# Performance work log

Hardware: AMD Instinct MI355X
Metric: run time of the kernel (lower is better)

## Reference

```python
import jax, jax.numpy as jnp
import numpy as np

L = 6        # gnn_layers
H = 4        # heads
C = 128      # per-head channels = hidden // heads
HID = 512    # hidden
IN = 768     # in_dim
N = 20000    # nodes
E = 320000   # edges
P = 100000   # scored pairs


def _gelu(v):
    return jax.nn.gelu(v, approximate=False)


def _ln(v, g, b):
    m = v.mean(-1, keepdims=True)
    var = v.var(-1, keepdims=True)
    return (v - m) / jnp.sqrt(var + 1e-5) * g + b


def setup_inputs() -> dict:
    key = jax.random.key(0)
    ks = jax.random.split(key, 24)
    g = lambda k, shape, s=0.02: (jax.random.normal(k, shape, jnp.float32) * s)
    inp = {}
    inp["x"] = jax.random.normal(ks[0], (N, IN), jnp.float32)
    inp["edge_index"] = jax.random.randint(ks[1], (2, E), 0, N)
    inp["edges"] = jax.random.randint(ks[2], (2, P), 0, N)
    # FeatureMixer (no alt branch)
    inp["mixer_W"] = g(ks[3], (IN, HID)); inp["mixer_b"] = jnp.zeros((HID,), jnp.float32)
    # Stacked TransformerConv params per layer
    inp["Wq"] = g(ks[4], (L, HID, HID)); inp["bq"] = jnp.zeros((L, HID), jnp.float32)
    inp["Wk"] = g(ks[5], (L, HID, HID)); inp["bk"] = jnp.zeros((L, HID), jnp.float32)
    inp["Wv"] = g(ks[6], (L, HID, HID)); inp["bv"] = jnp.zeros((L, HID), jnp.float32)
    inp["Ws"] = g(ks[7], (L, HID, HID)); inp["bs"] = jnp.zeros((L, HID), jnp.float32)  # lin_skip (root weight)
    inp["ln_g"] = jnp.ones((L, HID), jnp.float32); inp["ln_b"] = jnp.zeros((L, HID), jnp.float32)
    # Dual projections
    inp["syn_W"] = g(ks[8], (HID, HID)); inp["syn_b"] = jnp.zeros((HID,), jnp.float32)
    inp["ant_W"] = g(ks[9], (HID, HID)); inp["ant_b"] = jnp.zeros((HID,), jnp.float32)
    # Bilinear score matrices
    inp["W_syn"] = g(ks[10], (HID, HID), 0.04)
    inp["W_ant"] = g(ks[11], (HID, HID), 0.04)
    # Gate MLP: Linear(4*HID, HID) -> GELU -> Linear(HID, 1) -> Sigmoid
    inp["gW1"] = g(ks[12], (4 * HID, HID)); inp["gb1"] = jnp.zeros((HID,), jnp.float32)
    inp["gW2"] = g(ks[13], (HID, 1)); inp["gb2"] = jnp.zeros((1,), jnp.float32)
    return inp


def reference(x, edge_index, edges, mixer_W, mixer_b, Wq, bq, Wk, bk, Wv, bv,
              Ws, bs, ln_g, ln_b, syn_W, syn_b, ant_W, ant_b, W_syn, W_ant,
              gW1, gb1, gW2, gb2):
    src, dst = edge_index[0], edge_index[1]
    scale = 1.0 / np.sqrt(C).astype(np.float32)
    # FeatureMixer (eval mode: dropout = identity)
    h = _gelu(x @ mixer_W + mixer_b)  # [N, HID]
    for l in range(L):
        # node-side projections, then gather per edge
        q = (h @ Wq[l] + bq[l]).reshape(N, H, C)
        k = (h @ Wk[l] + bk[l]).reshape(N, H, C)
        v = (h @ Wv[l] + bv[l]).reshape(N, H, C)
        logits = (q[dst] * k[src]).sum(-1) * scale          # [E, H]
        mx = jax.ops.segment_max(logits, dst, num_segments=N)   # [N, H]
        ex = jnp.exp(logits - mx[dst])
        den = jax.ops.segment_sum(ex, dst, num_segments=N)      # [N, H]
        alpha = ex / den[dst]                                   # segment softmax over incoming edges
        msg = alpha[..., None] * v[src]                         # [E, H, C]
        out = jax.ops.segment_sum(msg, dst, num_segments=N).reshape(N, HID)
        out = out + h @ Ws[l] + bs[l]                           # root/skip term of TransformerConv
        out = _gelu(out)
        h = _ln(h + out, ln_g[l], ln_b[l])
    z_syn = _gelu(h @ syn_W + syn_b)
    z_ant = _gelu(h @ ant_W + ant_b)
    i, j = edges[0], edges[1]
    vi_s, vj_s = z_syn[i], z_syn[j]
    vi_a, vj_a = z_ant[i], z_ant[j]
    s_syn = ((vi_s @ W_syn) * vj_s).sum(-1)
    s_ant = ((vi_a @ W_ant) * vj_a).sum(-1)
    pair = jnp.concatenate([jnp.abs(vi_s - vj_s), vi_s * vj_s,
                            jnp.abs(vi_a - vj_a), vi_a * vj_a], axis=-1)  # [P, 4*HID]
    g = jax.nn.sigmoid(_gelu(pair @ gW1 + gb1) @ gW2 + gb2).squeeze(-1)
    return g * s_ant + (1.0 - g) * (-s_syn)
```

## Files before the change

### kernel.cpp

```cpp
#include <hip/hip_runtime.h>
#include <cstdint>

#define L_LAYERS 6

typedef __attribute__((ext_vector_type(8))) short bf16x8;
typedef __attribute__((ext_vector_type(4))) float f32x4;
typedef __attribute__((ext_vector_type(2))) float f32x2;

__device__ __forceinline__ float gelu1(float v) {
    return 0.5f * v * (1.0f + erff(v * 0.7071067811865475f));
}

__device__ __forceinline__ unsigned int f2bf2(float a, float b) {
    union { float f; unsigned u; } x, y;
    x.f = a; y.f = b;
    unsigned lo = (x.u + 0x7FFFu + ((x.u >> 16) & 1u)) >> 16;
    unsigned hi = (y.u + 0x7FFFu + ((y.u >> 16) & 1u)) & 0xFFFF0000u;
    return lo | hi;
}

__device__ __forceinline__ unsigned short f2bf1(float a) {
    union { float f; unsigned u; } x;
    x.f = a;
    return (unsigned short)((x.u + 0x7FFFu + ((x.u >> 16) & 1u)) >> 16);
}

__device__ __forceinline__ unsigned cvt_pk_bf16(float lo, float hi) {
    unsigned r;
    asm("v_cvt_pk_bf16_f32 %0, %1, %2" : "=v"(r) : "v"(lo), "v"(hi));
    return r;
}

__device__ __forceinline__ float2 bfp2(unsigned u) {
    union { unsigned u; float f; } a, b;
    a.u = u << 16;
    b.u = u & 0xFFFF0000u;
    return make_float2(a.f, b.f);
}

__device__ __forceinline__ void gload16(const void* g, void* l) {
    __builtin_amdgcn_global_load_lds(
        (const __attribute__((address_space(1))) void*)g,
        (__attribute__((address_space(3))) void*)l, 16, 0, 0);
}


__global__ void k_zero(int* __restrict__ p, int n) {
    int i = blockIdx.x * 256 + threadIdx.x;
    if (i < n) p[i] = 0;
}


__global__ void k_hist(const int* __restrict__ dst, int* __restrict__ hist, int E) {
    int e = blockIdx.x * 256 + threadIdx.x;
    if (e < E) atomicAdd(&hist[dst[e]], 1);
}

__global__ __launch_bounds__(1024) void k_scan(const int* __restrict__ hist,
                                               int* __restrict__ off, int n) {
    __shared__ int buf[1024];
    __shared__ int carry;
    int tid = threadIdx.x;
    if (tid == 0) carry = 0;
    __syncthreads();
    for (int base = 0; base < n; base += 1024) {
        int v = (base + tid < n) ? hist[base + tid] : 0;
        buf[tid] = v;
        __syncthreads();
        int x = v;
        for (int o = 1; o < 1024; o <<= 1) {
            int t = (tid >= o) ? buf[tid - o] : 0;
            __syncthreads();
            x += t;
            buf[tid] = x;
            __syncthreads();
        }
        int c = carry;
        if (base + tid < n) off[base + tid] = c + x - v;
        __syncthreads();
        if (tid == 1023) carry = c + buf[1023];
        __syncthreads();
    }
    if (tid == 0) off[n] = carry;
}

__global__ void k_scatter(const int* __restrict__ src, const int* __restrict__ dst,
                          const int* __restrict__ off, int* __restrict__ cursor,
                          int* __restrict__ srcS, int E) {
    int e = blockIdx.x * 256 + threadIdx.x;
    if (e < E) {
        int d = dst[e];
        int pos = off[d] + atomicAdd(&cursor[d], 1);
        srcS[pos] = src[e];
    }
}


__global__ void k_wcat(const float* __restrict__ Wq, const float* __restrict__ Wk,
                       const float* __restrict__ Wv, const float* __restrict__ Ws,
                       short* __restrict__ Wt) {
    int idx = blockIdx.x * 256 + threadIdx.x;
    int k = idx & 511;
    int nf = (idx >> 9) & 2047;
    int l = idx >> 20;
    int sel = nf >> 9, nn = nf & 511;
    const float* W = (sel == 0) ? Wq : (sel == 1) ? Wk : (sel == 2) ? Wv : Ws;
    float v = W[((size_t)l * 512 + k) * 512 + nn];
    Wt[idx] = (short)f2bf1(v);
}

__global__ void k_tr(const float* __restrict__ W, short* __restrict__ Wt, int K, int N,
                     int swz) {
    int k = blockIdx.x * 256 + threadIdx.x;
    int n = blockIdx.y;
    if (k < K) {
        int kk = k;
        if (swz) kk = (k & ~31) | (((((k >> 3) & 3) ^ ((n >> 1) & 3))) << 3) | (k & 7);
        Wt[(size_t)n * K + kk] = (short)f2bf1(W[(size_t)k * N + n]);
    }
}

__global__ void k_bcat(const float* __restrict__ bq, const float* __restrict__ bk,
                       const float* __restrict__ bv, const float* __restrict__ bs,
                       float* __restrict__ bcat) {
    int idx = blockIdx.x * 256 + threadIdx.x;
    if (idx >= L_LAYERS * 2048) return;
    int l = idx >> 11, n = idx & 2047;
    int sel = n >> 9, nn = n & 511;
    const float* b = (sel == 0) ? bq : (sel == 1) ? bk : (sel == 2) ? bv : bs;
    bcat[idx] = b[l * 512 + nn];
}

__global__ void k_bdual(const float* __restrict__ sb, const float* __restrict__ ab,
                        float* __restrict__ bd) {
    int idx = blockIdx.x * 256 + threadIdx.x;
    if (idx < 1024) bd[idx] = (idx < 512) ? sb[idx] : ab[idx - 512];
}


__global__ __launch_bounds__(256) void gemm_a32(
    const float* __restrict__ A, int lda,
    const short* __restrict__ Bt,
    const float* __restrict__ bias,
    float* __restrict__ Cf, short* __restrict__ Cbf, int ldc,
    int M, int N, int K, int act) {
    __shared__ __align__(16) short As[128][40];
    __shared__ __align__(16) short Bs[128][40];
    const int tid = threadIdx.x;
    const int lane = tid & 63;
    const int wave = tid >> 6;
    const int wr = (wave >> 1) * 64;
    const int wc = (wave & 1) * 64;
    const int l16 = lane & 15;
    const int quad = lane >> 4;
    const int row0 = blockIdx.x * 128;
    const int col0 = blockIdx.y * 128;
    const int sr = tid >> 2;
    const int sk = (tid & 3) * 8;

    f32x4 acc[4][4];
#pragma unroll
    for (int i = 0; i < 4; ++i)
#pragma unroll
        for (int j = 0; j < 4; ++j)
            acc[i][j] = f32x4{0.f, 0.f, 0.f, 0.f};

    for (int kb = 0; kb < K; kb += 32) {
#pragma unroll
        for (int hh = 0; hh < 2; ++hh) {
            int r = sr + hh * 64;
            int gr = row0 + r;
            float4 a0, a1;
            if (gr < M) {
                const float* p = A + (size_t)gr * lda + kb + sk;
                a0 = *(const float4*)p;
                a1 = *(const float4*)(p + 4);
            } else {
                a0 = make_float4(0.f, 0.f, 0.f, 0.f);
                a1 = make_float4(0.f, 0.f, 0.f, 0.f);
            }
            uint4 av;
            av.x = f2bf2(a0.x, a0.y);
            av.y = f2bf2(a0.z, a0.w);
            av.z = f2bf2(a1.x, a1.y);
            av.w = f2bf2(a1.z, a1.w);
            *(uint4*)&As[r][sk] = av;
            const short* bp = Bt + (size_t)(col0 + r) * K + kb + sk;
            *(uint4*)&Bs[r][sk] = *(const uint4*)bp;
        }
        __syncthreads();
        bf16x8 af[4], bfr[4];
#pragma unroll
        for (int i = 0; i < 4; ++i)
            af[i] = *(const bf16x8*)&As[wr + i * 16 + l16][quad * 8];
#pragma unroll
        for (int j = 0; j < 4; ++j)
            bfr[j] = *(const bf16x8*)&Bs[wc + j * 16 + l16][quad * 8];
#pragma unroll
        for (int i = 0; i < 4; ++i)
#pragma unroll
            for (int j = 0; j < 4; ++j)
                acc[i][j] = __builtin_amdgcn_mfma_f32_16x16x32_bf16(af[i], bfr[j], acc[i][j], 0, 0, 0);
        __syncthreads();
    }
#pragma unroll
    for (int i = 0; i < 4; ++i) {
        int rbase = row0 + wr + i * 16 + quad * 4;
#pragma unroll
        for (int j = 0; j < 4; ++j) {
            int c = col0 + wc + j * 16 + l16;
            float bv = bias ? bias[c] : 0.0f;
#pragma unroll
            for (int rg = 0; rg < 4; ++rg) {
                int gr = rbase + rg;
                if (gr < M) {
                    float v = acc[i][j][rg] + bv;
                    if (act) v = gelu1(v);
                    Cf[(size_t)gr * ldc + c] = v;
                    if (Cbf) Cbf[(size_t)gr * ldc + c] = (short)f2bf1(v);
                }
            }
        }
    }
}


__global__ __launch_bounds__(256) void gemm_bb(
    const short* __restrict__ A, int lda,
    const short* __restrict__ Bt,
    const float* __restrict__ bias,
    short* __restrict__ C, unsigned char* __restrict__ C8, int ldc,
    int M, int N, int K, int act) {
    __shared__ __align__(16) short As[128 * 32];
    __shared__ __align__(16) short Bs[128 * 32];
    const int tid = threadIdx.x;
    const int lane = tid & 63;
    const int wave = tid >> 6;
    const int wr = (wave >> 1) * 64;
    const int wc = (wave & 1) * 64;
    const int l16 = lane & 15;
    const int quad = lane >> 4;
    const int row0 = blockIdx.x * 128;
    const int col0 = blockIdx.y * 128;
    const int c0 = tid, c1 = tid + 256;
    const int r0 = c0 >> 2, kq0 = (c0 & 3) * 8;
    const int r1 = c1 >> 2, kq1 = (c1 & 3) * 8;
    int ga0 = row0 + r0; if (ga0 >= M) ga0 = M - 1;
    int ga1 = row0 + r1; if (ga1 >= M) ga1 = M - 1;
    const short* Ap0 = A + (size_t)ga0 * lda + kq0;
    const short* Ap1 = A + (size_t)ga1 * lda + kq1;
    const short* Bp0 = Bt + (size_t)(col0 + r0) * K + kq0;
    const short* Bp1 = Bt + (size_t)(col0 + r1) * K + kq1;

    f32x4 acc[4][4];
#pragma unroll
    for (int i = 0; i < 4; ++i)
#pragma unroll
        for (int j = 0; j < 4; ++j)
            acc[i][j] = f32x4{0.f, 0.f, 0.f, 0.f};

    for (int kb = 0; kb < K; kb += 32) {
        gload16(Ap0 + kb, &As[c0 * 8]);
        gload16(Ap1 + kb, &As[c1 * 8]);
        gload16(Bp0 + kb, &Bs[c0 * 8]);
        gload16(Bp1 + kb, &Bs[c1 * 8]);
        __syncthreads();
        bf16x8 af[4], bfr[4];
#pragma unroll
        for (int i = 0; i < 4; ++i)
            af[i] = *(const bf16x8*)&As[(wr + i * 16 + l16) * 32 + quad * 8];
#pragma unroll
        for (int j = 0; j < 4; ++j)
            bfr[j] = *(const bf16x8*)&Bs[(wc + j * 16 + l16) * 32 + quad * 8];
#pragma unroll
        for (int i = 0; i < 4; ++i)
#pragma unroll
            for (int j = 0; j < 4; ++j)
                acc[i][j] = __builtin_amdgcn_mfma_f32_16x16x32_bf16(af[i], bfr[j], acc[i][j], 0, 0, 0);
        __syncthreads();
    }
#pragma unroll
    for (int i = 0; i < 4; ++i) {
        int rbase = row0 + wr + i * 16 + quad * 4;
#pragma unroll
        for (int j = 0; j < 4; ++j) {
            int c = col0 + wc + j * 16 + l16;
            float bv = bias ? bias[c] : 0.0f;
#pragma unroll
            for (int rg = 0; rg < 4; ++rg) {
                int gr = rbase + rg;
                if (gr < M) {
                    float v = acc[i][j][rg] + bv;
                    if (act) v = gelu1(v);
                    C[(size_t)gr * ldc + c] = (short)f2bf1(v);
                    if (C8) {
                        int r8 = __builtin_amdgcn_cvt_pk_fp8_f32(v, v, 0, false);
                        C8[(size_t)gr * ldc + c] = (unsigned char)(r8 & 0xFF);
                    }
                }
            }
        }
    }
}


__global__ __launch_bounds__(256) void gemm_qkvs(
    const short* __restrict__ A,
    const short* __restrict__ Bt,
    const float* __restrict__ bias,
    short* __restrict__ qvs,
    unsigned char* __restrict__ kv8,
    int M, int mtiles) {
    const int K = 512;
    const int id = blockIdx.x;
    const int xcd = id & 7;
    const int t = id >> 3;
    const int col_t = t & 15;
    const int row_t = (t >> 4) * 8 + xcd;
    if (row_t >= mtiles) return;
    const int row0 = row_t * 128;
    const int col0 = col_t * 128;
    __shared__ __align__(16) short As[128 * 32];
    __shared__ __align__(16) short Bs[128 * 32];
    const int tid = threadIdx.x;
    const int lane = tid & 63;
    const int wave = tid >> 6;
    const int wr = (wave >> 1) * 64;
    const int wc = (wave & 1) * 64;
    const int l16 = lane & 15;
    const int quad = lane >> 4;
    const int c0 = tid, c1 = tid + 256;
    const int r0 = c0 >> 2, kq0 = (c0 & 3) * 8;
    const int r1 = c1 >> 2, kq1 = (c1 & 3) * 8;
    int ga0 = row0 + r0; if (ga0 >= M) ga0 = M - 1;
    int ga1 = row0 + r1; if (ga1 >= M) ga1 = M - 1;
    const short* Ap0 = A + (size_t)ga0 * K + kq0;
    const short* Ap1 = A + (size_t)ga1 * K + kq1;
    const short* Bp0 = Bt + (size_t)(col0 + r0) * K + kq0;
    const short* Bp1 = Bt + (size_t)(col0 + r1) * K + kq1;

    f32x4 acc[4][4];
#pragma unroll
    for (int i = 0; i < 4; ++i)
#pragma unroll
        for (int j = 0; j < 4; ++j)
            acc[i][j] = f32x4{0.f, 0.f, 0.f, 0.f};

    for (int kb = 0; kb < K; kb += 32) {
        gload16(Ap0 + kb, &As[c0 * 8]);
        gload16(Ap1 + kb, &As[c1 * 8]);
        gload16(Bp0 + kb, &Bs[c0 * 8]);
        gload16(Bp1 + kb, &Bs[c1 * 8]);
        __syncthreads();
        bf16x8 af[4], bfr[4];
#pragma unroll
        for (int i = 0; i < 4; ++i)
            af[i] = *(const bf16x8*)&As[(wr + i * 16 + l16) * 32 + quad * 8];
#pragma unroll
        for (int j = 0; j < 4; ++j)
            bfr[j] = *(const bf16x8*)&Bs[(wc + j * 16 + l16) * 32 + quad * 8];
#pragma unroll
        for (int i = 0; i < 4; ++i)
#pragma unroll
            for (int j = 0; j < 4; ++j)
                acc[i][j] = __builtin_amdgcn_mfma_f32_16x16x32_bf16(af[i], bfr[j], acc[i][j], 0, 0, 0);
        __syncthreads();
    }
#pragma unroll
    for (int i = 0; i < 4; ++i) {
        int rbase = row0 + wr + i * 16 + quad * 4;
#pragma unroll
        for (int j = 0; j < 4; ++j) {
            int c = col0 + wc + j * 16 + l16;
            int sec = c >> 9;
            int cc = c & 511;
            float bv = bias[c];
#pragma unroll
            for (int rg = 0; rg < 4; ++rg) {
                int gr = rbase + rg;
                if (gr < M) {
                    float v = acc[i][j][rg] + bv;
                    if (sec == 1 || sec == 2) {
                        int r8 = __builtin_amdgcn_cvt_pk_fp8_f32(v, v, 0, false);
                        int off = (sec == 1) ? cc : 512 + cc;
                        kv8[(size_t)gr * 1024 + off] = (unsigned char)(r8 & 0xFF);
                    } else {
                        int off = (sec == 0) ? cc : 512 + cc;
                        qvs[(size_t)gr * 1024 + off] = (short)f2bf1(v);
                    }
                }
            }
        }
    }
}


__global__ __launch_bounds__(512, 2) void gemm_gate(
    const unsigned char* __restrict__ z8,
    const int* __restrict__ pi, const int* __restrict__ pj, int P,
    const short* __restrict__ Bt,
    const float* __restrict__ gb1,
    const float* __restrict__ gW2,
    float* __restrict__ gpart) {
    __shared__ __align__(16) short Bs[512 * 32];
    __shared__ __align__(16) short As[128 * 32];
    __shared__ int iArr[128];
    __shared__ int jArr[128];
    __shared__ float rowsum[128];
    const int row0 = blockIdx.x * 128;
    const int tid = threadIdx.x;
    const int lane = tid & 63;
    const int wave = tid >> 6;
    const int wm = wave >> 2;
    const int wn = wave & 3;
    const int l16 = lane & 15;
    const int quad = lane >> 4;
    const int arow = tid >> 2;
    const int aslot = tid & 3;
    const int qs = (quad ^ ((l16 >> 1) & 3)) * 8;
    const int awoff = arow * 32 + ((aslot ^ ((arow >> 1) & 3)) << 3);

    if (tid < 128) {
        int p = row0 + tid;
        int ok = (p < P);
        iArr[tid] = ok ? pi[p] : 0;
        jArr[tid] = ok ? pj[p] : 0;
        rowsum[tid] = 0.0f;
    }
    __syncthreads();
    const unsigned char* zi = z8 + (size_t)iArr[arow] * 1024 + aslot * 8;
    const unsigned char* zj = z8 + (size_t)jArr[arow] * 1024 + aslot * 8;
    const short* brow = Bt + (size_t)(tid >> 2) * 2048 + (tid & 3) * 8;

    f32x4 acc[4][8];
#pragma unroll
    for (int i = 0; i < 4; ++i)
#pragma unroll
        for (int j = 0; j < 8; ++j)
            acc[i][j] = f32x4{0.f, 0.f, 0.f, 0.f};

    uint2 xu = *(const uint2*)zi;
    uint2 yu = *(const uint2*)zj;

    for (int kc = 0; kc < 32; ++kc) {
        const int chb = ((kc >> 4) << 10) + ((kc & 15) << 5);
#pragma unroll
        for (int g = 0; g < 4; ++g)
            gload16(brow + (size_t)(g * 128) * 2048 + chb, &Bs[(g * 512 + tid) * 8]);
        uint2 xn, yn;
        if (kc + 1 < 32) {
            int koff = (((kc + 1) >> 4) << 9) + (((kc + 1) & 15) << 5);
            xn = *(const uint2*)(zi + koff);
            yn = *(const uint2*)(zj + koff);
        }
        f32x2 x0 = __builtin_amdgcn_cvt_pk_f32_fp8((int)xu.x, false);
        f32x2 x1 = __builtin_amdgcn_cvt_pk_f32_fp8((int)xu.x, true);
        f32x2 x2 = __builtin_amdgcn_cvt_pk_f32_fp8((int)xu.y, false);
        f32x2 x3 = __builtin_amdgcn_cvt_pk_f32_fp8((int)xu.y, true);
        f32x2 y0 = __builtin_amdgcn_cvt_pk_f32_fp8((int)yu.x, false);
        f32x2 y1 = __builtin_amdgcn_cvt_pk_f32_fp8((int)yu.x, true);
        f32x2 y2 = __builtin_amdgcn_cvt_pk_f32_fp8((int)yu.y, false);
        f32x2 y3 = __builtin_amdgcn_cvt_pk_f32_fp8((int)yu.y, true);
        uint4 aa, am;
        aa.x = cvt_pk_bf16(fabsf(x0.x - y0.x), fabsf(x0.y - y0.y));
        aa.y = cvt_pk_bf16(fabsf(x1.x - y1.x), fabsf(x1.y - y1.y));
        aa.z = cvt_pk_bf16(fabsf(x2.x - y2.x), fabsf(x2.y - y2.y));
        aa.w = cvt_pk_bf16(fabsf(x3.x - y3.x), fabsf(x3.y - y3.y));
        am.x = cvt_pk_bf16(x0.x * y0.x, x0.y * y0.y);
        am.y = cvt_pk_bf16(x1.x * y1.x, x1.y * y1.y);
        am.z = cvt_pk_bf16(x2.x * y2.x, x2.y * y2.y);
        am.w = cvt_pk_bf16(x3.x * y3.x, x3.y * y3.y);
        *(uint4*)&As[awoff] = aa;
        __syncthreads();
        {
            bf16x8 af[4];
#pragma unroll
            for (int i = 0; i < 4; ++i)
                af[i] = *(const bf16x8*)&As[(wm * 64 + i * 16 + l16) * 32 + qs];
#pragma unroll
            for (int j = 0; j < 8; ++j) {
                bf16x8 bf = *(const bf16x8*)&Bs[(wn * 128 + j * 16 + l16) * 32 + qs];
#pragma unroll
                for (int i = 0; i < 4; ++i)
                    acc[i][j] = __builtin_amdgcn_mfma_f32_16x16x32_bf16(af[i], bf, acc[i][j], 0, 0, 0);
            }
        }
        __syncthreads();
#pragma unroll
        for (int g = 0; g < 4; ++g)
            gload16(brow + (size_t)(g * 128) * 2048 + chb + 512, &Bs[(g * 512 + tid) * 8]);
        *(uint4*)&As[awoff] = am;
        __syncthreads();
        {
            bf16x8 af[4];
#pragma unroll
            for (int i = 0; i < 4; ++i)
                af[i] = *(const bf16x8*)&As[(wm * 64 + i * 16 + l16) * 32 + qs];
#pragma unroll
            for (int j = 0; j < 8; ++j) {
                bf16x8 bf = *(const bf16x8*)&Bs[(wn * 128 + j * 16 + l16) * 32 + qs];
#pragma unroll
                for (int i = 0; i < 4; ++i)
                    acc[i][j] = __builtin_amdgcn_mfma_f32_16x16x32_bf16(af[i], bf, acc[i][j], 0, 0, 0);
            }
        }
        __syncthreads();
        xu = xn;
        yu = yn;
    }
#pragma unroll
    for (int i = 0; i < 4; ++i) {
#pragma unroll
        for (int rg = 0; rg < 4; ++rg) {
            float partial = 0.f;
#pragma unroll
            for (int j = 0; j < 8; ++j) {
                int cc = wn * 128 + j * 16 + l16;
                partial += gelu1(acc[i][j][rg] + gb1[cc]) * gW2[cc];
            }
            partial += __shfl_xor(partial, 1);
            partial += __shfl_xor(partial, 2);
            partial += __shfl_xor(partial, 4);
            partial += __shfl_xor(partial, 8);
            if (l16 == 0)
                atomicAdd(&rowsum[wm * 64 + i * 16 + quad * 4 + rg], partial);
        }
    }
    __syncthreads();
    if (tid < 128) {
        int p = row0 + tid;
        if (p < P) gpart[p] = rowsum[tid];
    }
}


__global__ __launch_bounds__(256) void k_attn(const short* __restrict__ qvs,
                                              const unsigned char* __restrict__ kv8,
                                              const int* __restrict__ srcS,
                                              const int* __restrict__ offs,
                                              float* __restrict__ h,
                                              short* __restrict__ h_bf,
                                              const float* __restrict__ lng,
                                              const float* __restrict__ lnb, int Nn) {
    const int tid = threadIdx.x;
    const int lane = tid & 63;
    const int wv = tid >> 6;
    const int n = blockIdx.x * 4 + wv;
    if (n >= Nn) return;
    const int st = offs[n], en = offs[n + 1];
    const size_t chOff = (size_t)lane * 8;

    uint4 qv = *(const uint4*)(qvs + (size_t)n * 1024 + chOff);
    float2 q0 = bfp2(qv.x), q1 = bfp2(qv.y), q2 = bfp2(qv.z), q3 = bfp2(qv.w);
    float acc[8];
#pragma unroll
    for (int i = 0; i < 8; ++i) acc[i] = 0.f;
    float m_l = -3.4e38f, l_l = 0.f;

    for (int e0 = st; e0 < en; e0 += 64) {
        int cnt = min(64, en - e0);
        int myS = (lane < cnt) ? srcS[e0 + lane] : 0;
        for (int ei = 0; ei < cnt; ++ei) {
            int s = __shfl(myS, ei);
            const unsigned char* srow = kv8 + (size_t)s * 1024 + chOff;
            uint2 kq = *(const uint2*)srow;
            uint2 vq = *(const uint2*)(srow + 512);
            f32x2 k0 = __builtin_amdgcn_cvt_pk_f32_fp8((int)kq.x, false);
            f32x2 k1 = __builtin_amdgcn_cvt_pk_f32_fp8((int)kq.x, true);
            f32x2 k2 = __builtin_amdgcn_cvt_pk_f32_fp8((int)kq.y, false);
            f32x2 k3 = __builtin_amdgcn_cvt_pk_f32_fp8((int)kq.y, true);
            float d = q0.x * k0.x + q0.y * k0.y + q1.x * k1.x + q1.y * k1.y +
                      q2.x * k2.x + q2.y * k2.y + q3.x * k3.x + q3.y * k3.y;
            d += __shfl_xor(d, 1);
            d += __shfl_xor(d, 2);
            d += __shfl_xor(d, 4);
            d += __shfl_xor(d, 8);
            float lg = d * 0.08838834764831845f;
            float m_new = fmaxf(m_l, lg);
            float sc = __expf(m_l - m_new);
            float p = __expf(lg - m_new);
            l_l = l_l * sc + p;
            m_l = m_new;
            f32x2 v0 = __builtin_amdgcn_cvt_pk_f32_fp8((int)vq.x, false);
            f32x2 v1 = __builtin_amdgcn_cvt_pk_f32_fp8((int)vq.x, true);
            f32x2 v2 = __builtin_amdgcn_cvt_pk_f32_fp8((int)vq.y, false);
            f32x2 v3 = __builtin_amdgcn_cvt_pk_f32_fp8((int)vq.y, true);
            acc[0] = acc[0] * sc + p * v0.x; acc[1] = acc[1] * sc + p * v0.y;
            acc[2] = acc[2] * sc + p * v1.x; acc[3] = acc[3] * sc + p * v1.y;
            acc[4] = acc[4] * sc + p * v2.x; acc[5] = acc[5] * sc + p * v2.y;
            acc[6] = acc[6] * sc + p * v3.x; acc[7] = acc[7] * sc + p * v3.y;
        }
    }
    float rinv = (en > st) ? 1.0f / l_l : 0.f;
    uint4 su = *(const uint4*)(qvs + (size_t)n * 1024 + 512 + chOff);
    float2 s0 = bfp2(su.x), s1 = bfp2(su.y), s2 = bfp2(su.z), s3 = bfp2(su.w);
    float sv[8] = {s0.x, s0.y, s1.x, s1.y, s2.x, s2.y, s3.x, s3.y};
    const float* hp = h + (size_t)n * 512 + chOff;
    float4 h0 = *(const float4*)hp;
    float4 h1 = *(const float4*)(hp + 4);
    float hv[8] = {h0.x, h0.y, h0.z, h0.w, h1.x, h1.y, h1.z, h1.w};
    float r[8];
    float sum = 0.f, ssq = 0.f;
#pragma unroll
    for (int i = 0; i < 8; ++i) {
        r[i] = hv[i] + gelu1(acc[i] * rinv + sv[i]);
        sum += r[i];
        ssq += r[i] * r[i];
    }
    for (int o = 32; o; o >>= 1) {
        sum += __shfl_xor(sum, o);
        ssq += __shfl_xor(ssq, o);
    }
    float mean = sum * (1.0f / 512.0f);
    float var = ssq * (1.0f / 512.0f) - mean * mean;
    float inv = rsqrtf(var + 1e-5f);
    const float* gp = lng + chOff;
    const float* bp = lnb + chOff;
    float4 g0 = *(const float4*)gp, g1 = *(const float4*)(gp + 4);
    float4 b0 = *(const float4*)bp, b1 = *(const float4*)(bp + 4);
    float ga[8] = {g0.x, g0.y, g0.z, g0.w, g1.x, g1.y, g1.z, g1.w};
    float ba[8] = {b0.x, b0.y, b0.z, b0.w, b1.x, b1.y, b1.z, b1.w};
    float o8[8];
#pragma unroll
    for (int i = 0; i < 8; ++i) o8[i] = (r[i] - mean) * inv * ga[i] + ba[i];
    float* hw = h + (size_t)n * 512 + chOff;
    *(float4*)hw = make_float4(o8[0], o8[1], o8[2], o8[3]);
    *(float4*)(hw + 4) = make_float4(o8[4], o8[5], o8[6], o8[7]);
    uint4 ob;
    ob.x = f2bf2(o8[0], o8[1]);
    ob.y = f2bf2(o8[2], o8[3]);
    ob.z = f2bf2(o8[4], o8[5]);
    ob.w = f2bf2(o8[6], o8[7]);
    *(uint4*)(h_bf + (size_t)n * 512 + chOff) = ob;
}


__global__ __launch_bounds__(256) void k_pairscore(const short* __restrict__ z,
                                                   const short* __restrict__ t,
                                                   const int* __restrict__ pi,
                                                   const int* __restrict__ pj,
                                                   float* __restrict__ ssyn,
                                                   float* __restrict__ sant, int P) {
    int p = blockIdx.x * 4 + (threadIdx.x >> 6);
    if (p >= P) return;
    int lane = threadIdx.x & 63;
    int i = pi[p], j = pj[p];
    uint4 a = *(const uint4*)(t + (size_t)i * 1024 + lane * 8);
    uint4 b = *(const uint4*)(z + (size_t)j * 1024 + lane * 8);
    float2 a0 = bfp2(a.x), a1 = bfp2(a.y), a2 = bfp2(a.z), a3 = bfp2(a.w);
    float2 b0 = bfp2(b.x), b1 = bfp2(b.y), b2 = bfp2(b.z), b3 = bfp2(b.w);
    float ds = a0.x * b0.x + a0.y * b0.y + a1.x * b1.x + a1.y * b1.y +
               a2.x * b2.x + a2.y * b2.y + a3.x * b3.x + a3.y * b3.y;
    uint4 c = *(const uint4*)(t + (size_t)i * 1024 + 512 + lane * 8);
    uint4 d = *(const uint4*)(z + (size_t)j * 1024 + 512 + lane * 8);
    float2 c0 = bfp2(c.x), c1 = bfp2(c.y), c2 = bfp2(c.z), c3 = bfp2(c.w);
    float2 d0 = bfp2(d.x), d1 = bfp2(d.y), d2 = bfp2(d.z), d3 = bfp2(d.w);
    float da = c0.x * d0.x + c0.y * d0.y + c1.x * d1.x + c1.y * d1.y +
               c2.x * d2.x + c2.y * d2.y + c3.x * d3.x + c3.y * d3.y;
    for (int o = 32; o; o >>= 1) {
        ds += __shfl_xor(ds, o);
        da += __shfl_xor(da, o);
    }
    if (lane == 0) { ssyn[p] = ds; sant[p] = da; }
}


__global__ void k_final(const float* __restrict__ gpart, const float* __restrict__ gb2,
                        const float* __restrict__ ssyn, const float* __restrict__ sant,
                        float* __restrict__ out, int P) {
    int p = blockIdx.x * 256 + threadIdx.x;
    if (p < P) {
        float s = 1.0f / (1.0f + __expf(-(gpart[p] + gb2[0])));
        out[p] = s * sant[p] - (1.0f - s) * ssyn[p];
    }
}


extern "C" void kernel_launch(void* const* d_in, const int* in_sizes, int n_in,
                              void* d_out, int out_size, void* d_ws, size_t ws_size,
                              hipStream_t stream) {
    const float* x = (const float*)d_in[0];
    const int* ei = (const int*)d_in[1];
    const int* pe = (const int*)d_in[2];
    const float* mixer_W = (const float*)d_in[3];
    const float* mixer_b = (const float*)d_in[4];
    const float* Wq = (const float*)d_in[5];
    const float* bq = (const float*)d_in[6];
    const float* Wk = (const float*)d_in[7];
    const float* bk = (const float*)d_in[8];
    const float* Wv = (const float*)d_in[9];
    const float* bv = (const float*)d_in[10];
    const float* Ws = (const float*)d_in[11];
    const float* bs = (const float*)d_in[12];
    const float* ln_g = (const float*)d_in[13];
    const float* ln_b = (const float*)d_in[14];
    const float* syn_W = (const float*)d_in[15];
    const float* syn_b = (const float*)d_in[16];
    const float* ant_W = (const float*)d_in[17];
    const float* ant_b = (const float*)d_in[18];
    const float* W_syn = (const float*)d_in[19];
    const float* W_ant = (const float*)d_in[20];
    const float* gW1 = (const float*)d_in[21];
    const float* gb1 = (const float*)d_in[22];
    const float* gW2 = (const float*)d_in[23];
    const float* gb2 = (const float*)d_in[24];
    float* out = (float*)d_out;

    const int Nn = in_sizes[0] / 768;
    const int E = in_sizes[1] / 2;
    const int P = in_sizes[2] / 2;

    char* w = (char*)d_ws;
    auto alloc = [&](size_t bytes) -> char* {
        char* p = w;
        w += (bytes + 255) & ~(size_t)255;
        return p;
    };
    float* h = (float*)alloc((size_t)Nn * 512 * 4);
    short* h_bf = (short*)alloc((size_t)Nn * 512 * 2);
    char* U = alloc((size_t)Nn * 2048 * 2);
    short* qvs = (short*)U;
    unsigned char* kv8 = (unsigned char*)(U + (size_t)Nn * 1024 * 2);
    short* zB = (short*)U;
    short* tB = (short*)(U + (size_t)Nn * 1024 * 2);
    unsigned char* z8 = (unsigned char*)alloc((size_t)Nn * 1024);
    float* ssyn = (float*)alloc((size_t)P * 3 * 4);
    float* sant = ssyn + P;
    float* gpart = ssyn + 2 * P;
    int* srcS = (int*)alloc((size_t)E * 4);
    int* hist = (int*)alloc((size_t)Nn * 2 * 4);
    int* cursor = hist + Nn;
    int* offs = (int*)alloc((size_t)(Nn + 1) * 4);
    short* mixWt = (short*)alloc((size_t)512 * 768 * 2);
    short* wcat = (short*)alloc((size_t)L_LAYERS * 2048 * 512 * 2);
    short* dualWt = (short*)alloc((size_t)1024 * 512 * 2);
    short* bilWt = (short*)alloc((size_t)1024 * 512 * 2);
    short* gw1t = (short*)alloc((size_t)512 * 2048 * 2);
    float* bcat = (float*)alloc((size_t)L_LAYERS * 2048 * 4);
    float* bdual = (float*)alloc((size_t)1024 * 4);

    k_zero<<<(2 * Nn + 255) / 256, 256, 0, stream>>>(hist, 2 * Nn);
    k_hist<<<(E + 255) / 256, 256, 0, stream>>>(ei + E, hist, E);
    k_scan<<<1, 1024, 0, stream>>>(hist, offs, Nn);
    k_scatter<<<(E + 255) / 256, 256, 0, stream>>>(ei, ei + E, offs, cursor, srcS, E);

    k_wcat<<<(L_LAYERS * 2048 * 512) / 256, 256, 0, stream>>>(Wq, Wk, Wv, Ws, wcat);
    k_tr<<<dim3(3, 512), 256, 0, stream>>>(mixer_W, mixWt, 768, 512, 0);
    k_tr<<<dim3(2, 512), 256, 0, stream>>>(syn_W, dualWt, 512, 512, 0);
    k_tr<<<dim3(2, 512), 256, 0, stream>>>(ant_W, dualWt + 512 * 512, 512, 512, 0);
    k_tr<<<dim3(2, 512), 256, 0, stream>>>(W_syn, bilWt, 512, 512, 0);
    k_tr<<<dim3(2, 512), 256, 0, stream>>>(W_ant, bilWt + 512 * 512, 512, 512, 0);
    k_tr<<<dim3(8, 512), 256, 0, stream>>>(gW1, gw1t, 2048, 512, 1);
    k_bcat<<<48, 256, 0, stream>>>(bq, bk, bv, bs, bcat);
    k_bdual<<<4, 256, 0, stream>>>(syn_b, ant_b, bdual);

    const int mtiles = (Nn + 127) / 128;
    gemm_a32<<<dim3(mtiles, 4), 256, 0, stream>>>(x, 768, mixWt, mixer_b, h, h_bf, 512,
                                                  Nn, 512, 768, 1);

    const int qk_grid = ((mtiles + 7) / 8) * 8 * 16;
    for (int l = 0; l < L_LAYERS; ++l) {
        gemm_qkvs<<<qk_grid, 256, 0, stream>>>(h_bf, wcat + (size_t)l * 2048 * 512,
                                               bcat + l * 2048, qvs, kv8, Nn, mtiles);
        k_attn<<<(Nn + 3) / 4, 256, 0, stream>>>(qvs, kv8, srcS, offs, h, h_bf,
                                                 ln_g + l * 512, ln_b + l * 512, Nn);
    }

    gemm_bb<<<dim3(mtiles, 8), 256, 0, stream>>>(h_bf, 512, dualWt, bdual, zB, z8, 1024,
                                                 Nn, 1024, 512, 1);
    gemm_bb<<<dim3(mtiles, 4), 256, 0, stream>>>(zB, 1024, bilWt, nullptr, tB, nullptr, 1024,
                                                 Nn, 512, 512, 0);
    gemm_bb<<<dim3(mtiles, 4), 256, 0, stream>>>(zB + 512, 1024, bilWt + 512 * 512, nullptr,
                                                 tB + 512, nullptr, 1024, Nn, 512, 512, 0);

    k_pairscore<<<(P + 3) / 4, 256, 0, stream>>>(zB, tB, pe, pe + P, ssyn, sant, P);

    const int ptiles2 = (P + 127) / 128;
    gemm_gate<<<ptiles2, 512, 0, stream>>>(z8, pe, pe + P, P, gw1t, gb1, gW2, gpart);
    k_final<<<(P + 255) / 256, 256, 0, stream>>>(gpart, gb2, ssyn, sant, out, P);
}
```

Baseline: 1.755 ms.

## Software-pipeline gate GEMM with double-buffered weight tiles and split A buffers

Restructures the gate-MLP GEMM main loop so the weight tile for the next phase is loaded into a second LDS buffer while the current phase runs its MFMAs. The absolute-difference and product A operands get separate LDS buffers, and the next chunk's fp8 conversion overlaps with compute. Explicit vmcnt waits plus raw s_barrier replace the four __syncthreads per iteration. The aim is to hide global-load latency and cut barrier stalls. LDS use per block rises to about 144KB, which likely allows only one block per CU and lowers occupancy.

```diff
diff --git a/kernel.cpp b/kernel.cpp
--- a/kernel.cpp
+++ b/kernel.cpp
@@ -402,8 +402,10 @@
     const float* __restrict__ gb1,
     const float* __restrict__ gW2,
     float* __restrict__ gpart) {
-    __shared__ __align__(16) short Bs[512 * 32];
-    __shared__ __align__(16) short As[128 * 32];
+    __shared__ __align__(16) short Bab[2 * 512 * 32];
+    __shared__ __align__(16) short Bmu[2 * 512 * 32];
+    __shared__ __align__(16) short Asab[128 * 32];
+    __shared__ __align__(16) short Asmu[128 * 32];
     __shared__ int iArr[128];
     __shared__ int jArr[128];
     __shared__ float rowsum[128];
@@ -439,20 +441,15 @@
         for (int j = 0; j < 8; ++j)
             acc[i][j] = f32x4{0.f, 0.f, 0.f, 0.f};
 
-    uint2 xu = *(const uint2*)zi;
-    uint2 yu = *(const uint2*)zj;
-
-    for (int kc = 0; kc < 32; ++kc) {
-        const int chb = ((kc >> 4) << 10) + ((kc & 15) << 5);
+    auto CHB = [](int kc) { return ((kc >> 4) << 10) + ((kc & 15) << 5); };
+    auto KOFF = [](int kc) { return ((kc >> 4) << 9) + ((kc & 15) << 5); };
+    auto STAGE = [&](int kc, int mu, short* buf) {
+        const short* src = brow + CHB(kc) + (mu ? 512 : 0);
 #pragma unroll
         for (int g = 0; g < 4; ++g)
-            gload16(brow + (size_t)(g * 128) * 2048 + chb, &Bs[(g * 512 + tid) * 8]);
-        uint2 xn, yn;
-        if (kc + 1 < 32) {
-            int koff = (((kc + 1) >> 4) << 9) + (((kc + 1) & 15) << 5);
-            xn = *(const uint2*)(zi + koff);
-            yn = *(const uint2*)(zj + koff);
-        }
+            gload16(src + (size_t)(g * 128) * 2048, buf + (g * 512 + tid) * 8);
+    };
+    auto CVT = [&](uint2 xu, uint2 yu, uint4& aa, uint4& am) {
         f32x2 x0 = __builtin_amdgcn_cvt_pk_f32_fp8((int)xu.x, false);
         f32x2 x1 = __builtin_amdgcn_cvt_pk_f32_fp8((int)xu.x, true);
         f32x2 x2 = __builtin_amdgcn_cvt_pk_f32_fp8((int)xu.y, false);
@@ -461,7 +458,6 @@
         f32x2 y1 = __builtin_amdgcn_cvt_pk_f32_fp8((int)yu.x, true);
         f32x2 y2 = __builtin_amdgcn_cvt_pk_f32_fp8((int)yu.y, false);
         f32x2 y3 = __builtin_amdgcn_cvt_pk_f32_fp8((int)yu.y, true);
-        uint4 aa, am;
         aa.x = cvt_pk_bf16(fabsf(x0.x - y0.x), fabsf(x0.y - y0.y));
         aa.y = cvt_pk_bf16(fabsf(x1.x - y1.x), fabsf(x1.y - y1.y));
         aa.z = cvt_pk_bf16(fabsf(x2.x - y2.x), fabsf(x2.y - y2.y));
@@ -470,44 +466,56 @@
         am.y = cvt_pk_bf16(x1.x * y1.x, x1.y * y1.y);
         am.z = cvt_pk_bf16(x2.x * y2.x, x2.y * y2.y);
         am.w = cvt_pk_bf16(x3.x * y3.x, x3.y * y3.y);
-        *(uint4*)&As[awoff] = aa;
-        __syncthreads();
-        {
-            bf16x8 af[4];
+    };
+    auto MFMA_PHASE = [&](const short* As, const short* Bp) {
+        bf16x8 af[4];
+#pragma unroll
+        for (int i = 0; i < 4; ++i)
+            af[i] = *(const bf16x8*)&As[(wm * 64 + i * 16 + l16) * 32 + qs];
+#pragma unroll
+        for (int j = 0; j < 8; ++j) {
+            bf16x8 bf = *(const bf16x8*)&Bp[(wn * 128 + j * 16 + l16) * 32 + qs];
 #pragma unroll
             for (int i = 0; i < 4; ++i)
-                af[i] = *(const bf16x8*)&As[(wm * 64 + i * 16 + l16) * 32 + qs];
-#pragma unroll
-            for (int j = 0; j < 8; ++j) {
-                bf16x8 bf = *(const bf16x8*)&Bs[(wn * 128 + j * 16 + l16) * 32 + qs];
-#pragma unroll
-                for (int i = 0; i < 4; ++i)
-                    acc[i][j] = __builtin_amdgcn_mfma_f32_16x16x32_bf16(af[i], bf, acc[i][j], 0, 0, 0);
-            }
+                acc[i][j] = __builtin_amdgcn_mfma_f32_16x16x32_bf16(af[i], bf, acc[i][j], 0, 0, 0);
         }
-        __syncthreads();
-#pragma unroll
-        for (int g = 0; g < 4; ++g)
-            gload16(brow + (size_t)(g * 128) * 2048 + chb + 512, &Bs[(g * 512 + tid) * 8]);
-        *(uint4*)&As[awoff] = am;
-        __syncthreads();
-        {
-            bf16x8 af[4];
-#pragma unroll
-            for (int i = 0; i < 4; ++i)
-                af[i] = *(const bf16x8*)&As[(wm * 64 + i * 16 + l16) * 32 + qs];
-#pragma unroll
-            for (int j = 0; j < 8; ++j) {
-                bf16x8 bf = *(const bf16x8*)&Bs[(wn * 128 + j * 16 + l16) * 32 + qs];
-#pragma unroll
-                for (int i = 0; i < 4; ++i)
-                    acc[i][j] = __builtin_amdgcn_mfma_f32_16x16x32_bf16(af[i], bf, acc[i][j], 0, 0, 0);
-            }
-        }
-        __syncthreads();
-        xu = xn;
-        yu = yn;
-    }
+    };
+
+    STAGE(0, 0, Bab);
+    uint2 xu = *(const uint2*)zi;
+    uint2 yu = *(const uint2*)zj;
+    uint4 aa, am, am_hold;
+    CVT(xu, yu, aa, am);
+    *(uint4*)&Asab[awoff] = aa;
+    am_hold = am;
+
+#pragma unroll 1
+    for (int kc = 0; kc < 31; ++kc) {
+        const int cur = kc & 1;
+        STAGE(kc, 1, Bmu + cur * 16384);
+        uint2 xn = *(const uint2*)(zi + KOFF(kc + 1));
+        uint2 yn = *(const uint2*)(zj + KOFF(kc + 1));
+        asm volatile("s_waitcnt vmcnt(6) lgkmcnt(0)" ::: "memory");
+        __builtin_amdgcn_s_barrier();
+        MFMA_PHASE(Asab, Bab + cur * 16384);
+        *(uint4*)&Asmu[awoff] = am_hold;
+        STAGE(kc + 1, 0, Bab + (cur ^ 1) * 16384);
+        CVT(xn, yn, aa, am);
+        asm volatile("s_waitcnt vmcnt(4) lgkmcnt(0)" ::: "memory");
+        __builtin_amdgcn_s_barrier();
+        MFMA_PHASE(Asmu, Bmu + cur * 16384);
+        *(uint4*)&Asab[awoff] = aa;
+        am_hold = am;
+    }
+    STAGE(31, 1, Bmu + 16384);
+    asm volatile("s_waitcnt vmcnt(4) lgkmcnt(0)" ::: "memory");
+    __builtin_amdgcn_s_barrier();
+    MFMA_PHASE(Asab, Bab + 16384);
+    *(uint4*)&Asmu[awoff] = am_hold;
+    asm volatile("s_waitcnt vmcnt(0) lgkmcnt(0)" ::: "memory");
+    __builtin_amdgcn_s_barrier();
+    MFMA_PHASE(Asmu, Bmu + 16384);
+
 #pragma unroll
     for (int i = 0; i < 4; ++i) {
 #pragma unroll
```

New measurement: 1.660 ms. -5.4%, faster.
